# Kernel tuning notes

Measured on AMD Instinct MI355X. Metric: run time of the kernel, lower is better.

Reference implementation:

```python
import jax, jax.numpy as jnp
import numpy as np
from math import sqrt

D_MODEL = 1024
N_HEADS = 16
D_T = 256
D_HID = 4 * D_MODEL
EPS = 1e-6


def _rmsnorm(x):
    # RMSNorm without affine: x / sqrt(mean(x^2) + eps)
    return x * jax.lax.rsqrt(jnp.mean(x * x, axis=-1, keepdims=True) + EPS)


def setup_inputs() -> dict:
    key = jax.random.key(0)
    ks = jax.random.split(key, 16)
    s = 0.02  # weight init scale
    inp = {
        "x": jax.random.normal(ks[0], (4, 2048, D_MODEL), dtype=jnp.float32),
        "t": jax.random.normal(ks[1], (4, D_T), dtype=jnp.float32),
        # AdaRMSNorm (attn) : Linear(d_t, d_model, bias=False) weights stored (out, in)
        "attn_gamma_w": jax.random.normal(ks[2], (D_MODEL, D_T), dtype=jnp.float32) * s,
        "attn_beta_w": jax.random.normal(ks[3], (D_MODEL, D_T), dtype=jnp.float32) * s,
        # Attention projections
        "W_q": jax.random.normal(ks[4], (D_MODEL, D_MODEL), dtype=jnp.float32) * s,
        "W_k": jax.random.normal(ks[5], (D_MODEL, D_MODEL), dtype=jnp.float32) * s,
        "W_v": jax.random.normal(ks[6], (D_MODEL, D_MODEL), dtype=jnp.float32) * s,
        "W_o": jax.random.normal(ks[7], (D_MODEL, D_MODEL), dtype=jnp.float32) * s,
        "attn_alpha_w": jax.random.normal(ks[8], (D_MODEL, D_T), dtype=jnp.float32) * s,
        # AdaRMSNorm (ffn)
        "ffn_gamma_w": jax.random.normal(ks[9], (D_MODEL, D_T), dtype=jnp.float32) * s,
        "ffn_beta_w": jax.random.normal(ks[10], (D_MODEL, D_T), dtype=jnp.float32) * s,
        # SwiGLU
        "gate_w": jax.random.normal(ks[11], (D_HID, D_MODEL), dtype=jnp.float32) * s,
        "hidden_w": jax.random.normal(ks[12], (D_HID, D_MODEL), dtype=jnp.float32) * s,
        "out_w": jax.random.normal(ks[13], (D_MODEL, D_HID), dtype=jnp.float32) * s,
        "out_b": jnp.zeros((D_MODEL,), dtype=jnp.float32),
        "ffn_alpha_w": jax.random.normal(ks[14], (D_MODEL, D_T), dtype=jnp.float32) * s,
    }
    return inp


def _ada_rmsnorm(x, t, gamma_w, beta_w):
    gamma = (t @ gamma_w.T)[:, None, :]  # [b, 1, d]
    beta = (t @ beta_w.T)[:, None, :]
    return gamma * _rmsnorm(x) + beta


def _attention(x, W_q, W_k, W_v, W_o):
    b, l, dm = x.shape
    d_head = dm // N_HEADS
    scale = sqrt(N_HEADS / dm)  # == 1/sqrt(d_head)
    def split(y):  # [b, l, dm] -> [b, n, l, d]
        return y.reshape(b, l, N_HEADS, d_head).transpose(0, 2, 1, 3)
    q = split(x @ W_q.T)
    k = split(x @ W_k.T)
    v = split(x @ W_v.T)
    attn = jax.nn.softmax(scale * jnp.einsum("bnqd,bnkd->bnqk", q, k), axis=-1)
    o = jnp.einsum("bnqk,bnkd->bnqd", attn, v)
    o = o.transpose(0, 2, 1, 3).reshape(b, l, dm)
    return o @ W_o.T


def _swiglu(x, gate_w, hidden_w, out_w, out_b):
    return (jax.nn.silu(x @ gate_w.T) * (x @ hidden_w.T)) @ out_w.T + out_b


def reference(x, t, attn_gamma_w, attn_beta_w, W_q, W_k, W_v, W_o, attn_alpha_w,
              ffn_gamma_w, ffn_beta_w, gate_w, hidden_w, out_w, out_b, ffn_alpha_w):
    a_alpha = (t @ attn_alpha_w.T)[:, None, :]
    x = x + a_alpha * _attention(_ada_rmsnorm(x, t, attn_gamma_w, attn_beta_w), W_q, W_k, W_v, W_o)
    f_alpha = (t @ ffn_alpha_w.T)[:, None, :]
    return x + f_alpha * _swiglu(_ada_rmsnorm(x, t, ffn_gamma_w, ffn_beta_w), gate_w, hidden_w, out_w, out_b)
```

## Files before the change

### kernel.cpp

```cpp
#include <hip/hip_runtime.h>
#include <hip/hip_bf16.h>

typedef __attribute__((ext_vector_type(8))) short short8;
typedef __attribute__((ext_vector_type(4))) short short4v;
typedef __attribute__((ext_vector_type(4))) float f32x4;
using bf16 = __hip_bfloat16;
using lds_bf16 = __attribute__((address_space(3))) bf16;

#define BARF()  asm volatile("s_barrier" ::: "memory")
#define LGKM0() asm volatile("s_waitcnt lgkmcnt(0)" ::: "memory")
#define VMC4()  asm volatile("s_waitcnt vmcnt(4)" ::: "memory")
#define VMC2()  asm volatile("s_waitcnt vmcnt(2)" ::: "memory")
#define VMC0()  asm volatile("s_waitcnt vmcnt(0)" ::: "memory")
#define SCHED0() __builtin_amdgcn_sched_barrier(0)
#define PRIO1() __builtin_amdgcn_s_setprio(1)
#define PRIO0() __builtin_amdgcn_s_setprio(0)

static __device__ __forceinline__ short bfb(float f) {
  bf16 h = __float2bfloat16(f);
  short r; __builtin_memcpy(&r, &h, 2); return r;
}

static __device__ __forceinline__ void gld_lds16(const bf16* g, bf16* l) {
  __builtin_amdgcn_global_load_lds(
      (const __attribute__((address_space(1))) void*)g,
      (__attribute__((address_space(3))) void*)l, 16, 0, 0);
}

static __device__ __forceinline__ short8 dsr(const lds_bf16* b, int imm) {
  short8 v;
  asm volatile("ds_read_b128 %0, %1 offset:%2" : "=v"(v) : "v"(b), "i"(imm));
  return v;
}

__global__ __launch_bounds__(256) void cvt_all_kernel(
    const float* __restrict__ s0, const float* __restrict__ s1, const float* __restrict__ s2,
    const float* __restrict__ s3, const float* __restrict__ gw, const float* __restrict__ hw,
    const float* __restrict__ ow, bf16* __restrict__ dbase) {
  size_t c = (size_t)blockIdx.x * 256 + threadIdx.x;
  const float* src; size_t se;
  if (c < 524288) {
    int seg = (int)(c >> 17);
    src = (seg == 0) ? s0 : (seg == 1) ? s1 : (seg == 2) ? s2 : s3;
    se = (c - ((size_t)seg << 17)) * 8;
  } else if (c < 1572864) {
    size_t lc = c - 524288;
    size_t row = lc >> 7;
    src = (row & 1) ? hw : gw;
    se = ((row >> 1) << 10) + ((lc & 127) << 3);
  } else { src = ow; se = (c - 1572864) * 8; }
  float4 v0 = *(const float4*)(src + se);
  float4 v1 = *(const float4*)(src + se + 4);
  short8 o;
  o[0] = bfb(v0.x); o[1] = bfb(v0.y); o[2] = bfb(v0.z); o[3] = bfb(v0.w);
  o[4] = bfb(v1.x); o[5] = bfb(v1.y); o[6] = bfb(v1.z); o[7] = bfb(v1.w);
  *(short8*)(dbase + c * 8) = o;
}

__global__ __launch_bounds__(256) void tproj_kernel(const float* __restrict__ t,
    const float* __restrict__ w0, const float* __restrict__ w1, const float* __restrict__ w2,
    const float* __restrict__ w3, const float* __restrict__ w4, const float* __restrict__ w5,
    float* __restrict__ out) {
  int gid = blockIdx.x * 256 + threadIdx.x;
  int s = gid >> 12, rem = gid & 4095;
  int b = rem >> 10, n = rem & 1023;
  const float* w = (s == 0) ? w0 : (s == 1) ? w1 : (s == 2) ? w2 : (s == 3) ? w3 : (s == 4) ? w4 : w5;
  const float4* tv = (const float4*)(t + b * 256);
  const float4* wv = (const float4*)(w + n * 256);
  float acc = 0.f;
  #pragma unroll 8
  for (int j = 0; j < 64; ++j) {
    float4 a = tv[j], c = wv[j];
    acc += a.x * c.x + a.y * c.y + a.z * c.z + a.w * c.w;
  }
  out[gid] = acc;
}

__global__ __launch_bounds__(256) void ada_rms_kernel(const float* __restrict__ x,
    const float* __restrict__ gamma, const float* __restrict__ beta, bf16* __restrict__ out) {
  int row = blockIdx.x;
  int b = row >> 11;
  int tid = threadIdx.x;
  const float* xr = x + (size_t)row * 1024;
  float4 v = *(const float4*)(xr + tid * 4);
  float ss = v.x * v.x + v.y * v.y + v.z * v.z + v.w * v.w;
  #pragma unroll
  for (int m = 1; m < 64; m <<= 1) ss += __shfl_xor(ss, m);
  __shared__ float red[4];
  if ((tid & 63) == 0) red[tid >> 6] = ss;
  __syncthreads();
  float tot = red[0] + red[1] + red[2] + red[3];
  float rinv = rsqrtf(tot * (1.0f / 1024.0f) + 1e-6f);
  const float* g  = gamma + b * 1024 + tid * 4;
  const float* be = beta  + b * 1024 + tid * 4;
  short4v o;
  o[0] = bfb(g[0] * v.x * rinv + be[0]);
  o[1] = bfb(g[1] * v.y * rinv + be[1]);
  o[2] = bfb(g[2] * v.z * rinv + be[2]);
  o[3] = bfb(g[3] * v.w * rinv + be[3]);
  *(short4v*)(out + (size_t)row * 1024 + tid * 4) = o;
}

enum { EPI8_GH = 1, EPI8_FIN = 2 };

#define RDA_M(d, mh) { \
  _Pragma("unroll") for (int mq = 0; mq < 4; ++mq) { \
    a[mq][0] = dsr(aB0, (d) * 32768 + ((mh) * 4 + mq) * 2048); \
    a[mq][1] = dsr(aB1, (d) * 32768 + ((mh) * 4 + mq) * 2048); } }
#define RDB0_M(d, nh) { \
  _Pragma("unroll") for (int nq = 0; nq < 2; ++nq) { \
    b0[nq][0] = dsr(bB0, (d) * 32768 + ((nh) * 2 + nq) * 2048); \
    b0[nq][1] = dsr(bB1, (d) * 32768 + ((nh) * 2 + nq) * 2048); } }
#define RDB1_M(d, nh) { \
  _Pragma("unroll") for (int nq = 0; nq < 2; ++nq) { \
    b1[nq][0] = dsr(bB0, (d) * 32768 + ((nh) * 2 + nq) * 2048); \
    b1[nq][1] = dsr(bB1, (d) * 32768 + ((nh) * 2 + nq) * 2048); } }
#define RDB0_F(d) { b0[0][0] = dsr(bB0, (d) * 16384); b0[0][1] = dsr(bB1, (d) * 16384); }
#define RDB1_F(d) { b1[0][0] = dsr(bB0, (d) * 16384 + 2048); b1[0][1] = dsr(bB1, (d) * 16384 + 2048); }

template<int EPI, int BN>
__global__ __launch_bounds__(512, 2) void gemm8p_kernel(
    const bf16* __restrict__ A, const bf16* __restrict__ B,
    int N, int K,
    bf16* __restrict__ o1, float* __restrict__ outF,
    const float* __restrict__ aux1, const float* __restrict__ aux2,
    const float* __restrict__ bias)
{
  constexpr int SB_ELEMS = (BN == 256) ? (2 * 2 * 128 * 64) : (2 * 128 * 64);
  __shared__ __align__(16) bf16 sA[2 * 2 * 128 * 64];
  __shared__ __align__(16) bf16 sB[SB_ELEMS];
  const int tid = threadIdx.x;
  const int lane = tid & 63, w = tid >> 6;
  const int wr = w >> 2, wcn = w & 3;
  const int bid = (int)blockIdx.x;
  const int ntn = (BN == 256) ? (N >> 8) : (N >> 7);
  const int trow = (bid / ntn) << 8;
  const int tcol = (bid % ntn) * BN;
  const int fr = lane & 15, hi = lane >> 4;
  const int rbase = hi << 2;
  const int NITER = K >> 7;
  const int st_row = (w << 4) + (lane >> 3);
  const int st_col = (((lane & 7) ^ ((lane >> 3) & 7)) << 3);
  const bf16* AsH0 = A + (size_t)(trow + st_row) * K + st_col;
  const bf16* AsH1 = AsH0 + (size_t)128 * K;
  const bf16* BsH0 = B + (size_t)(tcol + st_row) * K + st_col;
  const bf16* BsH1 = BsH0 + (size_t)128 * K;
  const size_t K8 = (size_t)K << 3;
  bf16* dA = sA + (w << 10);
  bf16* dB = sB + (w << 10);

  auto stA = [&](int dbuf, int h, int t) {
    const bf16* s = (h ? AsH1 : AsH0) + (t << 6);
    bf16* d = dA + ((dbuf * 2 + h) << 13);
    gld_lds16(s, d);
    gld_lds16(s + K8, d + 512);
  };
  auto stB2 = [&](int dbuf, int h, int t) {
    const bf16* s = (h ? BsH1 : BsH0) + (t << 6);
    bf16* d = dB + ((dbuf * 2 + h) << 13);
    gld_lds16(s, d);
    gld_lds16(s + K8, d + 512);
  };
  auto stB1 = [&](int dbuf, int t) {
    const bf16* s = BsH0 + (t << 6);
    bf16* d = dB + (dbuf << 13);
    gld_lds16(s, d);
    gld_lds16(s + K8, d + 512);
  };
  const int colK0 = (hi << 3) ^ ((fr & 7) << 3);
  const int colK1 = (32 + (hi << 3)) ^ ((fr & 7) << 3);
  const lds_bf16* aB0 = (const lds_bf16*)(sA + (wr << 13) + (fr << 6) + colK0);
  const lds_bf16* aB1 = (const lds_bf16*)(sA + (wr << 13) + (fr << 6) + colK1);
  const lds_bf16 *bB0, *bB1;
  if constexpr (BN == 256) {
    bB0 = (const lds_bf16*)(sB + ((wcn >> 1) << 13) + ((wcn & 1) << 12) + (fr << 6) + colK0);
    bB1 = (const lds_bf16*)(sB + ((wcn >> 1) << 13) + ((wcn & 1) << 12) + (fr << 6) + colK1);
  } else {
    bB0 = (const lds_bf16*)(sB + (wcn << 11) + (fr << 6) + colK0);
    bB1 = (const lds_bf16*)(sB + (wcn << 11) + (fr << 6) + colK1);
  }

  f32x4 acc[8][BN / 64] = {};
  short8 a[4][2], b0[2][2], b1[2][2];

  if constexpr (BN == 256) {
    auto QUAD0 = [&](int mh, int nh) {
      #pragma unroll
      for (int kk = 0; kk < 2; ++kk)
        #pragma unroll
        for (int mq = 0; mq < 4; ++mq)
          #pragma unroll
          for (int nq = 0; nq < 2; ++nq)
            acc[mh * 4 + mq][nh * 2 + nq] = __builtin_amdgcn_mfma_f32_16x16x32_bf16(
                a[mq][kk], b0[nq][kk], acc[mh * 4 + mq][nh * 2 + nq], 0, 0, 0);
    };
    auto QUAD1 = [&](int mh, int nh) {
      #pragma unroll
      for (int kk = 0; kk < 2; ++kk)
        #pragma unroll
        for (int mq = 0; mq < 4; ++mq)
          #pragma unroll
          for (int nq = 0; nq < 2; ++nq)
            acc[mh * 4 + mq][nh * 2 + nq] = __builtin_amdgcn_mfma_f32_16x16x32_bf16(
                a[mq][kk], b1[nq][kk], acc[mh * 4 + mq][nh * 2 + nq], 0, 0, 0);
    };
    stB2(0, 0, 0); stB2(0, 1, 0); stA(0, 0, 0); stA(0, 1, 0);
    stB2(1, 0, 1); stB2(1, 1, 1);
    VMC4();
    BARF();
    for (int i = 0; i < NITER; ++i) {
      const int t1 = 2 * i + 1, tn0 = 2 * i + 2, tn1 = 2 * i + 3;
      const bool g = (i != NITER - 1);
      RDA_M(0, 0); RDB0_M(0, 0);
      stA(1, 0, t1);
      BARF(); LGKM0(); SCHED0(); PRIO1(); QUAD0(0, 0); PRIO0(); BARF();
      RDB1_M(0, 1);
      stA(1, 1, t1);
      BARF(); LGKM0(); SCHED0(); PRIO1(); QUAD1(0, 1); PRIO0(); BARF();
      RDA_M(0, 1);
      if (g) stB2(0, 0, tn0);
      BARF(); LGKM0(); SCHED0(); PRIO1(); QUAD1(1, 1); PRIO0(); BARF();
      if (g) stB2(0, 1, tn0);
      BARF(); LGKM0(); SCHED0(); PRIO1(); QUAD0(1, 0); PRIO0();
      if (g) { VMC4(); } else { VMC0(); }
      BARF();
      RDA_M(1, 0); RDB0_M(1, 0);
      if (g) stA(0, 0, tn0);
      BARF(); LGKM0(); SCHED0(); PRIO1(); QUAD0(0, 0); PRIO0(); BARF();
      RDB1_M(1, 1);
      if (g) stA(0, 1, tn0);
      BARF(); LGKM0(); SCHED0(); PRIO1(); QUAD1(0, 1); PRIO0(); BARF();
      RDA_M(1, 1);
      if (g) stB2(1, 0, tn1);
      BARF(); LGKM0(); SCHED0(); PRIO1(); QUAD1(1, 1); PRIO0(); BARF();
      if (g) stB2(1, 1, tn1);
      BARF(); LGKM0(); SCHED0(); PRIO1(); QUAD0(1, 0); PRIO0();
      if (g) { VMC4(); }
      BARF();
    }
  } else {
    auto QUADF0 = [&](int mh) {
      #pragma unroll
      for (int kk = 0; kk < 2; ++kk)
        #pragma unroll
        for (int mq = 0; mq < 4; ++mq)
          acc[mh * 4 + mq][0] = __builtin_amdgcn_mfma_f32_16x16x32_bf16(
              a[mq][kk], b0[0][kk], acc[mh * 4 + mq][0], 0, 0, 0);
    };
    auto QUADF1 = [&](int mh) {
      #pragma unroll
      for (int kk = 0; kk < 2; ++kk)
        #pragma unroll
        for (int mq = 0; mq < 4; ++mq)
          acc[mh * 4 + mq][1] = __builtin_amdgcn_mfma_f32_16x16x32_bf16(
              a[mq][kk], b1[0][kk], acc[mh * 4 + mq][1], 0, 0, 0);
    };
    stB1(0, 0); stA(0, 0, 0); stA(0, 1, 0); stB1(1, 1);
    VMC2();
    BARF();
    for (int i = 0; i < NITER; ++i) {
      const int t1 = 2 * i + 1, tn0 = 2 * i + 2, tn1 = 2 * i + 3;
      const bool g = (i != NITER - 1);
      RDA_M(0, 0); RDB0_F(0);
      stA(1, 0, t1);
      BARF(); LGKM0(); SCHED0(); PRIO1(); QUADF0(0); PRIO0(); BARF();
      RDB1_F(0);
      stA(1, 1, t1);
      BARF(); LGKM0(); SCHED0(); PRIO1(); QUADF1(0); PRIO0(); BARF();
      RDA_M(0, 1);
      if (g) stB1(0, tn0);
      BARF(); LGKM0(); SCHED0(); PRIO1(); QUADF1(1); PRIO0(); BARF();
      BARF(); LGKM0(); SCHED0(); PRIO1(); QUADF0(1); PRIO0();
      if (g) { VMC2(); } else { VMC0(); }
      BARF();
      RDA_M(1, 0); RDB0_F(1);
      if (g) stA(0, 0, tn0);
      BARF(); LGKM0(); SCHED0(); PRIO1(); QUADF0(0); PRIO0(); BARF();
      RDB1_F(1);
      if (g) stA(0, 1, tn0);
      BARF(); LGKM0(); SCHED0(); PRIO1(); QUADF1(0); PRIO0(); BARF();
      RDA_M(1, 1);
      if (g) stB1(1, tn1);
      BARF(); LGKM0(); SCHED0(); PRIO1(); QUADF1(1); PRIO0(); BARF();
      BARF(); LGKM0(); SCHED0(); PRIO1(); QUADF0(1); PRIO0();
      if (g) { VMC2(); }
      BARF();
    }
  }

  #pragma unroll
  for (int m = 0; m < 8; ++m)
  #pragma unroll
  for (int n = 0; n < BN / 64; ++n)
  #pragma unroll
  for (int r = 0; r < 4; ++r) {
    int row = trow + (wr << 7) + m * 16 + rbase + r;
    int col = tcol + wcn * (BN / 4) + n * 16 + fr;
    float c = acc[m][n][r];
    if constexpr (EPI == EPI8_GH) {
      float other = __shfl_xor(c, 1);
      if (!(fr & 1)) {
        float sg = c / (1.f + __expf(-c));
        o1[(size_t)row * 4096 + (col >> 1)] = __float2bfloat16(sg * other);
      }
    } else {
      int b = row >> 11;
      size_t idx = (size_t)row * 1024 + col;
      outF[idx] = aux1[idx] + aux2[b * 1024 + col] * (c + bias[col]);
    }
  }
}

enum { EPI_RESID = 0, EPI_QKV3 = 2 };

template<int EPI>
__global__ __launch_bounds__(256) void gemm_bt_kernel(
    const bf16* __restrict__ A, const bf16* __restrict__ B,
    int N, int K,
    float* __restrict__ outF,
    const float* __restrict__ aux1, const float* __restrict__ aux2,
    bf16* __restrict__ oq, bf16* __restrict__ okk, bf16* __restrict__ ovt)
{
  __shared__ __align__(16) bf16 As[128][32];
  __shared__ __align__(16) bf16 Bs[128][32];
  const int tid = threadIdx.x;
  const int lane = tid & 63, wid = tid >> 6;
  const int wr = wid >> 1, wc = wid & 1;
  const int bid = (int)blockIdx.x;
  const int ntn = N >> 7;
  const int trow = (bid / ntn) << 7;
  const int tcol = (bid % ntn) << 7;
  const int fr = lane & 15, fc = (lane >> 4) << 3;
  const int rbase = (lane >> 4) << 2;
  const bf16* gA0 = A + (size_t)(trow + wid * 32 + (lane >> 2)) * K + ((lane & 3) << 3);
  const bf16* gA1 = gA0 + (size_t)16 * K;
  const bf16* gB0 = B + (size_t)(tcol + wid * 32 + (lane >> 2)) * K + ((lane & 3) << 3);
  const bf16* gB1 = gB0 + (size_t)16 * K;
  bf16* lA0 = &As[wid * 32][0];
  bf16* lA1 = &As[wid * 32 + 16][0];
  bf16* lB0 = &Bs[wid * 32][0];
  bf16* lB1 = &Bs[wid * 32 + 16][0];
  f32x4 acc[4][4] = {};
  for (int k0 = 0; k0 < K; k0 += 32) {
    __syncthreads();
    gld_lds16(gA0 + k0, lA0);
    gld_lds16(gA1 + k0, lA1);
    gld_lds16(gB0 + k0, lB0);
    gld_lds16(gB1 + k0, lB1);
    __syncthreads();
    short8 af[4], bfr[4];
    #pragma unroll
    for (int m = 0; m < 4; ++m) af[m] = *(const short8*)&As[wr * 64 + m * 16 + fr][fc];
    #pragma unroll
    for (int n = 0; n < 4; ++n) bfr[n] = *(const short8*)&Bs[wc * 64 + n * 16 + fr][fc];
    #pragma unroll
    for (int m = 0; m < 4; ++m)
      #pragma unroll
      for (int n = 0; n < 4; ++n)
        acc[m][n] = __builtin_amdgcn_mfma_f32_16x16x32_bf16(af[m], bfr[n], acc[m][n], 0, 0, 0);
  }
  if constexpr (EPI == EPI_QKV3) {
    #pragma unroll
    for (int m = 0; m < 4; ++m)
    #pragma unroll
    for (int n = 0; n < 4; ++n) {
      int row0 = trow + wr * 64 + m * 16 + rbase;
      int col  = tcol + wc * 64 + n * 16 + fr;
      int seg = col >> 10, cc = col & 1023;
      int bb = row0 >> 11, h2 = cc >> 6, dd = cc & 63;
      if (seg == 0) {
        #pragma unroll
        for (int r = 0; r < 4; ++r) {
          int l = (row0 + r) & 2047;
          oq[(((size_t)(bb * 16 + h2) * 2048 + l) << 6) + dd] =
              __float2bfloat16(acc[m][n][r] * 0.18033688f);
        }
      } else if (seg == 1) {
        #pragma unroll
        for (int r = 0; r < 4; ++r) {
          int l = (row0 + r) & 2047;
          okk[(((size_t)(bb * 16 + h2) * 2048 + l) << 6) + dd] = __float2bfloat16(acc[m][n][r]);
        }
      } else {
        int l = row0 & 2047;
        short4v o4;
        #pragma unroll
        for (int r = 0; r < 4; ++r) o4[r] = bfb(acc[m][n][r]);
        *(short4v*)&ovt[(((size_t)(bb * 16 + h2) * 64 + dd) << 11) + l] = o4;
      }
    }
  } else {
    #pragma unroll
    for (int m = 0; m < 4; ++m)
    #pragma unroll
    for (int n = 0; n < 4; ++n)
    #pragma unroll
    for (int r = 0; r < 4; ++r) {
      int row = trow + wr * 64 + m * 16 + rbase + r;
      int col = tcol + wc * 64 + n * 16 + fr;
      int b = row >> 11;
      size_t idx = (size_t)row * 1024 + col;
      outF[idx] = aux1[idx] + aux2[b * 1024 + col] * acc[m][n][r];
    }
  }
}

__global__ __launch_bounds__(512, 4) void attn_kernel(const bf16* __restrict__ q,
    const bf16* __restrict__ k, const bf16* __restrict__ vt, bf16* __restrict__ o) {
  const int id = blockIdx.x;
  const int bh = id & 63;
  const int qt = id >> 6;
  const int b = bh >> 4, h = bh & 15;
  __shared__ __align__(16) bf16 Ks[2][64][72];
  __shared__ __align__(16) bf16 Vs[2][64][72];
  __shared__ __align__(16) bf16 Ps[256][72];
  const int tid = threadIdx.x, lane = tid & 63, w = tid >> 6;
  const int fr = lane & 15, hi = lane >> 4;
  const int fc = hi << 3, rbase = hi << 2;
  const bf16* qbase = q + ((size_t)bh * 2048 + qt * 256) * 64;
  const bf16* kbase = k + (size_t)bh * 2048 * 64;
  const bf16* vbase = vt + (size_t)bh * 64 * 2048;
  short8 qf[2][2];
  #pragma unroll
  for (int nq = 0; nq < 2; ++nq)
    #pragma unroll
    for (int ks = 0; ks < 2; ++ks)
      qf[nq][ks] = *(const short8*)(qbase + (size_t)(w * 32 + nq * 16 + fr) * 64 + ks * 32 + fc);
  short8 onesf;
  #pragma unroll
  for (int j = 0; j < 8; ++j) onesf[j] = (short)0x3F80;
  f32x4 accO[4][2] = {};
  f32x4 accD[2] = {};
  const int sr = tid >> 3, sc = (tid & 7) << 3;
  *(short8*)&Ks[0][sr][sc] = *(const short8*)(kbase + (size_t)sr * 64 + sc);
  *(short8*)&Vs[0][sr][sc] = *(const short8*)(vbase + (size_t)sr * 2048 + sc);
  short8 rk = *(const short8*)(kbase + (size_t)(64 + sr) * 64 + sc);
  short8 rv = *(const short8*)(vbase + (size_t)sr * 2048 + 64 + sc);
  __syncthreads();
  for (int kt = 0; kt < 2048; kt += 64) {
    const int cur = (kt >> 6) & 1;
    f32x4 s[4][2] = {};
    #pragma unroll
    for (int ks = 0; ks < 2; ++ks) {
      short8 kf[4];
      #pragma unroll
      for (int mk = 0; mk < 4; ++mk) kf[mk] = *(const short8*)&Ks[cur][mk * 16 + fr][ks * 32 + fc];
      #pragma unroll
      for (int mk = 0; mk < 4; ++mk)
        #pragma unroll
        for (int nq = 0; nq < 2; ++nq)
          s[mk][nq] = __builtin_amdgcn_mfma_f32_16x16x32_bf16(kf[mk], qf[nq][ks], s[mk][nq], 0, 0, 0);
    }
    if (kt + 64 < 2048) {
      *(short8*)&Ks[cur ^ 1][sr][sc] = rk;
      *(short8*)&Vs[cur ^ 1][sr][sc] = rv;
      if (kt + 128 < 2048) {
        rk = *(const short8*)(kbase + (size_t)(kt + 128 + sr) * 64 + sc);
        rv = *(const short8*)(vbase + (size_t)sr * 2048 + kt + 128 + sc);
      }
    }
    #pragma unroll
    for (int mk = 0; mk < 4; ++mk)
      #pragma unroll
      for (int nq = 0; nq < 2; ++nq) {
        short4v pk;
        pk[0] = bfb(exp2f(s[mk][nq][0]));
        pk[1] = bfb(exp2f(s[mk][nq][1]));
        pk[2] = bfb(exp2f(s[mk][nq][2]));
        pk[3] = bfb(exp2f(s[mk][nq][3]));
        *(short4v*)&Ps[w * 32 + nq * 16 + fr][mk * 16 + rbase] = pk;
      }
    #pragma unroll
    for (int ks2 = 0; ks2 < 2; ++ks2) {
      short8 av[4], bp[2];
      #pragma unroll
      for (int nd = 0; nd < 4; ++nd) av[nd] = *(const short8*)&Vs[cur][nd * 16 + fr][ks2 * 32 + fc];
      #pragma unroll
      for (int nq = 0; nq < 2; ++nq) bp[nq] = *(const short8*)&Ps[w * 32 + nq * 16 + fr][ks2 * 32 + fc];
      #pragma unroll
      for (int nd = 0; nd < 4; ++nd)
        #pragma unroll
        for (int nq = 0; nq < 2; ++nq)
          accO[nd][nq] = __builtin_amdgcn_mfma_f32_16x16x32_bf16(av[nd], bp[nq], accO[nd][nq], 0, 0, 0);
      #pragma unroll
      for (int nq = 0; nq < 2; ++nq)
        accD[nq] = __builtin_amdgcn_mfma_f32_16x16x32_bf16(onesf, bp[nq], accD[nq], 0, 0, 0);
    }
    LGKM0(); BARF();
  }
  float rd[2];
  #pragma unroll
  for (int nq = 0; nq < 2; ++nq) rd[nq] = 1.0f / accD[nq][0];
  #pragma unroll
  for (int nd = 0; nd < 4; ++nd)
    #pragma unroll
    for (int nq = 0; nq < 2; ++nq) {
      short4v ov;
      #pragma unroll
      for (int r = 0; r < 4; ++r) ov[r] = bfb(accO[nd][nq][r] * rd[nq]);
      int qrow = qt * 256 + w * 32 + nq * 16 + fr;
      int col = h * 64 + nd * 16 + rbase;
      *(short4v*)&o[((size_t)b * 2048 + qrow) * 1024 + col] = ov;
    }
}

extern "C" void kernel_launch(void* const* d_in, const int* in_sizes, int n_in,
                              void* d_out, int out_size, void* d_ws, size_t ws_size,
                              hipStream_t stream) {
  (void)in_sizes; (void)n_in; (void)out_size; (void)ws_size;
  const float* x   = (const float*)d_in[0];
  const float* t   = (const float*)d_in[1];
  const float* agw = (const float*)d_in[2];
  const float* abw = (const float*)d_in[3];
  const float* wq  = (const float*)d_in[4];
  const float* wk  = (const float*)d_in[5];
  const float* wv  = (const float*)d_in[6];
  const float* wo  = (const float*)d_in[7];
  const float* aaw = (const float*)d_in[8];
  const float* fgw = (const float*)d_in[9];
  const float* fbw = (const float*)d_in[10];
  const float* gw  = (const float*)d_in[11];
  const float* hw  = (const float*)d_in[12];
  const float* ow  = (const float*)d_in[13];
  const float* ob  = (const float*)d_in[14];
  const float* faw = (const float*)d_in[15];
  float* out = (float*)d_out;

  char* p = (char*)d_ws;
  auto alloc = [&](size_t bytes) -> char* {
    char* r = p; p += (bytes + 255) & ~(size_t)255; return r;
  };
  float* tp    = (float*)alloc((size_t)6 * 4096 * 4);
  bf16* wq_b   = (bf16*)alloc((size_t)1024 * 1024 * 2);
  bf16* wk_b   = (bf16*)alloc((size_t)1024 * 1024 * 2);
  bf16* wv_b   = (bf16*)alloc((size_t)1024 * 1024 * 2);
  bf16* wo_b   = (bf16*)alloc((size_t)1024 * 1024 * 2);
  bf16* wgh_b  = (bf16*)alloc((size_t)8192 * 1024 * 2);
  bf16* wout_b = (bf16*)alloc((size_t)1024 * 4096 * 2);
  bf16* xn_b   = (bf16*)alloc((size_t)8192 * 1024 * 2);
  bf16* q_b    = (bf16*)alloc((size_t)8192 * 1024 * 2);
  bf16* k_b    = (bf16*)alloc((size_t)8192 * 1024 * 2);
  bf16* vt_b   = (bf16*)alloc((size_t)8192 * 1024 * 2);
  bf16* ao_b   = (bf16*)alloc((size_t)8192 * 1024 * 2);
  float* xmid  = (float*)alloc((size_t)8192 * 1024 * 4);
  bf16* gh_b   = (bf16*)alloc((size_t)8192 * 4096 * 2);

  cvt_all_kernel<<<8192, 256, 0, stream>>>(wq, wk, wv, wo, gw, hw, ow, wq_b);
  tproj_kernel<<<96, 256, 0, stream>>>(t, agw, abw, aaw, fgw, fbw, faw, tp);
  ada_rms_kernel<<<8192, 256, 0, stream>>>(x, tp + 0 * 4096, tp + 1 * 4096, xn_b);
  gemm_bt_kernel<EPI_QKV3><<<1536, 256, 0, stream>>>(xn_b, wq_b, 3072, 1024,
      nullptr, nullptr, nullptr, q_b, k_b, vt_b);
  attn_kernel<<<512, 512, 0, stream>>>(q_b, k_b, vt_b, ao_b);
  gemm_bt_kernel<EPI_RESID><<<512, 256, 0, stream>>>(ao_b, wo_b, 1024, 1024, xmid, x, tp + 2 * 4096, nullptr, nullptr, nullptr);
  ada_rms_kernel<<<8192, 256, 0, stream>>>(xmid, tp + 3 * 4096, tp + 4 * 4096, xn_b);
  gemm8p_kernel<EPI8_GH, 256><<<1024, 512, 0, stream>>>(xn_b, wgh_b, 8192, 1024, gh_b, nullptr, nullptr, nullptr, nullptr);
  gemm8p_kernel<EPI8_FIN, 128><<<256, 512, 0, stream>>>(gh_b, wout_b, 1024, 4096, nullptr, out, xmid, tp + 5 * 4096, ob);
}
```

Baseline: 522.3 us.

## Load K and V fragments directly from global memory in attention kernel

The attention kernel no longer stages K and V tiles through double-buffered shared memory with register prefetch. Each wave now reads its MFMA K and V operands straight from global memory (relying on L1/L2 caching), and the per-iteration barrier is removed. This frees LDS and drops the synchronisation, which may allow more occupancy. The cost is that every one of the 8 waves re-reads the same K/V data from cache with no software prefetch, so global-load latency sits directly before the MFMAs.

```diff
diff --git a/kernel.cpp b/kernel.cpp
--- a/kernel.cpp
+++ b/kernel.cpp
@@ -411,8 +411,6 @@
   const int bh = id & 63;
   const int qt = id >> 6;
   const int b = bh >> 4, h = bh & 15;
-  __shared__ __align__(16) bf16 Ks[2][64][72];
-  __shared__ __align__(16) bf16 Vs[2][64][72];
   __shared__ __align__(16) bf16 Ps[256][72];
   const int tid = threadIdx.x, lane = tid & 63, w = tid >> 6;
   const int fr = lane & 15, hi = lane >> 4;
@@ -431,34 +429,19 @@
   for (int j = 0; j < 8; ++j) onesf[j] = (short)0x3F80;
   f32x4 accO[4][2] = {};
   f32x4 accD[2] = {};
-  const int sr = tid >> 3, sc = (tid & 7) << 3;
-  *(short8*)&Ks[0][sr][sc] = *(const short8*)(kbase + (size_t)sr * 64 + sc);
-  *(short8*)&Vs[0][sr][sc] = *(const short8*)(vbase + (size_t)sr * 2048 + sc);
-  short8 rk = *(const short8*)(kbase + (size_t)(64 + sr) * 64 + sc);
-  short8 rv = *(const short8*)(vbase + (size_t)sr * 2048 + 64 + sc);
-  __syncthreads();
+  const bf16* kfb = kbase + (size_t)fr * 64 + fc;
+  const bf16* vfb = vbase + (size_t)fr * 2048;
   for (int kt = 0; kt < 2048; kt += 64) {
-    const int cur = (kt >> 6) & 1;
     f32x4 s[4][2] = {};
     #pragma unroll
-    for (int ks = 0; ks < 2; ++ks) {
-      short8 kf[4];
-      #pragma unroll
-      for (int mk = 0; mk < 4; ++mk) kf[mk] = *(const short8*)&Ks[cur][mk * 16 + fr][ks * 32 + fc];
-      #pragma unroll
-      for (int mk = 0; mk < 4; ++mk)
+    for (int ks = 0; ks < 2; ++ks)
+      #pragma unroll
+      for (int mk = 0; mk < 4; ++mk) {
+        short8 kf = *(const short8*)(kfb + (size_t)(kt + mk * 16) * 64 + ks * 32);
         #pragma unroll
         for (int nq = 0; nq < 2; ++nq)
-          s[mk][nq] = __builtin_amdgcn_mfma_f32_16x16x32_bf16(kf[mk], qf[nq][ks], s[mk][nq], 0, 0, 0);
-    }
-    if (kt + 64 < 2048) {
-      *(short8*)&Ks[cur ^ 1][sr][sc] = rk;
-      *(short8*)&Vs[cur ^ 1][sr][sc] = rv;
-      if (kt + 128 < 2048) {
-        rk = *(const short8*)(kbase + (size_t)(kt + 128 + sr) * 64 + sc);
-        rv = *(const short8*)(vbase + (size_t)sr * 2048 + kt + 128 + sc);
+          s[mk][nq] = __builtin_amdgcn_mfma_f32_16x16x32_bf16(kf, qf[nq][ks], s[mk][nq], 0, 0, 0);
       }
-    }
     #pragma unroll
     for (int mk = 0; mk < 4; ++mk)
       #pragma unroll
@@ -474,7 +457,8 @@
     for (int ks2 = 0; ks2 < 2; ++ks2) {
       short8 av[4], bp[2];
       #pragma unroll
-      for (int nd = 0; nd < 4; ++nd) av[nd] = *(const short8*)&Vs[cur][nd * 16 + fr][ks2 * 32 + fc];
+      for (int nd = 0; nd < 4; ++nd)
+        av[nd] = *(const short8*)(vfb + (size_t)(nd * 16) * 2048 + kt + ks2 * 32 + fc);
       #pragma unroll
       for (int nq = 0; nq < 2; ++nq) bp[nq] = *(const short8*)&Ps[w * 32 + nq * 16 + fr][ks2 * 32 + fc];
       #pragma unroll
@@ -486,7 +470,6 @@
       for (int nq = 0; nq < 2; ++nq)
         accD[nq] = __builtin_amdgcn_mfma_f32_16x16x32_bf16(onesf, bp[nq], accD[nq], 0, 0, 0);
     }
-    LGKM0(); BARF();
   }
   float rd[2];
   #pragma unroll
```

Result: slower. 652.1 us (+24.9%).
